# Kernel optimization log

Hardware: AMD Instinct MI355X
Metric: run time of the kernel (lower is better)

Reference implementation:

```python
import jax, jax.numpy as jnp
import numpy as np

B, S = 128, 72
ITER = 16
D_MODEL, D_INPUT = 1024, 512
MEM = 25
HEADS, DH = 8, 64
N_SO, N_SA = 256, 64
NUM_CLASSES = 1968
MH = 16
VOCAB, TED = 32, 128
SA_SZ = N_SA * (N_SA + 1) // 2  # 2080
SO_SZ = N_SO * (N_SO + 1) // 2  # 32896
I_A, J_A = np.triu_indices(N_SA)
I_O, J_O = np.triu_indices(N_SO)


def _ln(x, g, b):
    m = x.mean(-1, keepdims=True)
    v = ((x - m) ** 2).mean(-1, keepdims=True)
    return (x - m) / jnp.sqrt(v + 1e-5) * g + b


def _glu(x):
    a, g = jnp.split(x, 2, axis=-1)
    return a * jax.nn.sigmoid(g)


def setup_inputs():
    key = jax.random.key(0)
    ks = iter(jax.random.split(key, 32))

    def u(shape, s):
        return jax.random.uniform(next(ks), shape, jnp.float32, -s, s)

    return {
        "x": jax.random.randint(next(ks), (B, S), 0, VOCAB),
        "emb": u((VOCAB, TED), 1.0),
        "kv_w": u((TED, D_INPUT), (1.0 / TED) ** 0.5),
        "kv_b": jnp.zeros((D_INPUT,), jnp.float32),
        "kv_ln_g": jnp.ones((D_INPUT,), jnp.float32),
        "kv_ln_b": jnp.zeros((D_INPUT,), jnp.float32),
        "q_w": u((SA_SZ, D_INPUT), (1.0 / SA_SZ) ** 0.5),
        "q_b": jnp.zeros((D_INPUT,), jnp.float32),
        "in_proj_w": u((D_INPUT, 3 * D_INPUT), (1.0 / D_INPUT) ** 0.5),
        "in_proj_b": jnp.zeros((3 * D_INPUT,), jnp.float32),
        "out_proj_w": u((D_INPUT, D_INPUT), (1.0 / D_INPUT) ** 0.5),
        "out_proj_b": jnp.zeros((D_INPUT,), jnp.float32),
        "syn_w": u((D_INPUT + D_MODEL, 2 * D_MODEL), (1.0 / (D_INPUT + D_MODEL)) ** 0.5),
        "syn_b": jnp.zeros((2 * D_MODEL,), jnp.float32),
        "syn_ln_g": jnp.ones((D_MODEL,), jnp.float32),
        "syn_ln_b": jnp.zeros((D_MODEL,), jnp.float32),
        "tp1_w": u((MEM, 2 * MH, D_MODEL), 1.0 / (MEM + 2 * MH) ** 0.5),
        "tp1_b": jnp.zeros((1, D_MODEL, 2 * MH), jnp.float32),
        "tp2_w": u((MH, 2, D_MODEL), 1.0 / (MH + 2) ** 0.5),
        "tp2_b": jnp.zeros((1, D_MODEL, 2), jnp.float32),
        "start_act": u((D_MODEL,), (1.0 / D_MODEL) ** 0.5),
        "start_trace": u((D_MODEL, MEM), (1.0 / (D_MODEL + MEM)) ** 0.5),
        "decay_action": jnp.zeros((SA_SZ,), jnp.float32),
        "decay_out": jnp.zeros((SO_SZ,), jnp.float32),
        "out_w": u((SO_SZ, NUM_CLASSES), (1.0 / SO_SZ) ** 0.5),
        "out_b": jnp.zeros((NUM_CLASSES,), jnp.float32),
    }


def _forward(x, emb, kv_w, kv_b, kv_ln_g, kv_ln_b, q_w, q_b, in_proj_w, in_proj_b,
             out_proj_w, out_proj_b, syn_w, syn_b, syn_ln_g, syn_ln_b,
             tp1_w, tp1_b, tp2_w, tp2_b, start_act, start_trace,
             decay_action, decay_out, out_w, out_b):
    Bn = x.shape[0]
    # kv features: embed -> linear -> layernorm  (B,S,D_INPUT)
    kv = _ln(emb[x] @ kv_w + kv_b, kv_ln_g, kv_ln_b)
    Wq, Wk, Wv = jnp.split(in_proj_w, 3, axis=1)
    bq, bk, bv = jnp.split(in_proj_b, 3, axis=0)
    K = (kv @ Wk + bk).reshape(Bn, -1, HEADS, DH)  # (B,S,H,Dh)
    V = (kv @ Wv + bv).reshape(Bn, -1, HEADS, DH)
    # decayed running-sync coefficients (decay params clamped to [0,15])
    r_a = jnp.exp(-jnp.clip(decay_action, 0.0, 15.0))
    r_o = jnp.exp(-jnp.clip(decay_out, 0.0, 15.0))
    act0 = jnp.broadcast_to(start_act, (Bn, D_MODEL))
    trace0 = jnp.broadcast_to(start_trace, (Bn, D_MODEL, MEM))
    so0 = act0[:, :N_SO]
    a_o0 = so0[:, I_O] * so0[:, J_O]           # initial out-sync alpha
    b_o0 = jnp.ones_like(a_o0)
    a_a0 = jnp.zeros((Bn, SA_SZ), kv.dtype)    # None-init == zeros under update rule
    b_a0 = jnp.zeros((Bn, SA_SZ), kv.dtype)

    def step(carry, _):
        act, trace, a_a, b_a, a_o, b_o = carry
        # action synchronisation (last N_SA neurons, triu outer product)
        sa = act[:, -N_SA:]
        a_a = r_a * a_a + sa[:, I_A] * sa[:, J_A]
        b_a = r_a * b_a + 1.0
        sync_a = a_a / jnp.sqrt(b_a)
        # single-query multihead attention over kv
        q = sync_a @ q_w + q_b
        qh = (q @ Wq + bq).reshape(Bn, HEADS, DH)
        scores = jnp.einsum('bhd,bshd->bhs', qh, K) / (DH ** 0.5)
        attn = jax.nn.softmax(scores, axis=-1)
        o = jnp.einsum('bhs,bshd->bhd', attn, V).reshape(Bn, D_INPUT)
        o = o @ out_proj_w + out_proj_b
        # synapses: concat -> linear -> GLU -> layernorm
        pre = jnp.concatenate([o, act], axis=-1)
        state = _ln(_glu(pre @ syn_w + syn_b), syn_ln_g, syn_ln_b)
        # shift trace, append new state
        trace = jnp.concatenate([trace[:, :, 1:], state[:, :, None]], axis=-1)
        # per-neuron NLM: SuperLinear -> GLU -> SuperLinear -> GLU -> squeeze
        h = _glu(jnp.einsum('bdm,mhd->bdh', trace, tp1_w) + tp1_b)      # (B,D,MH)
        act = _glu(jnp.einsum('bdm,mhd->bdh', h, tp2_w) + tp2_b)[..., 0]  # (B,D)
        # out synchronisation (first N_SO neurons)
        so = act[:, :N_SO]
        a_o = r_o * a_o + so[:, I_O] * so[:, J_O]
        b_o = r_o * b_o + 1.0
        sync_o = a_o / jnp.sqrt(b_o)
        pred = sync_o @ out_w + out_b                                   # (B,C)
        lp = jax.nn.log_softmax(pred, axis=-1)
        ne = -jnp.sum(jnp.exp(lp) * lp, axis=-1) / jnp.log(jnp.float32(NUM_CLASSES))
        cert = jnp.stack([ne, 1.0 - ne], axis=-1)                       # (B,2)
        return (act, trace, a_a, b_a, a_o, b_o), (pred, cert)

    _, (preds, certs) = jax.lax.scan(step, (act0, trace0, a_a0, b_a0, a_o0, b_o0), None, length=ITER)
    predictions = jnp.moveaxis(preds, 0, -1)   # (B,C,ITER)
    certainties = jnp.moveaxis(certs, 0, -1)   # (B,2,ITER)
    return predictions, certainties


def reference(x, emb, kv_w, kv_b, kv_ln_g, kv_ln_b, q_w, q_b, in_proj_w, in_proj_b,
              out_proj_w, out_proj_b, syn_w, syn_b, syn_ln_g, syn_ln_b,
              tp1_w, tp1_b, tp2_w, tp2_b, start_act, start_trace,
              decay_action, decay_out, out_w, out_b):
    return _forward(x, emb, kv_w, kv_b, kv_ln_g, kv_ln_b, q_w, q_b, in_proj_w, in_proj_b,
                    out_proj_w, out_proj_b, syn_w, syn_b, syn_ln_g, syn_ln_b,
                    tp1_w, tp1_b, tp2_w, tp2_b, start_act, start_trace,
                    decay_action, decay_out, out_w, out_b)
```

## Files before the change

kernel.cpp:

```cpp
#include <hip/hip_runtime.h>
#include <math.h>

#define BB 128
#define SS 72
#define NITER 16
#define D_IN 512
#define D_MODEL 1024
#define MEMN 25
#define HEADS 8
#define DHH 64
#define N_SO 256
#define N_SA 64
#define SA_SZ 2080
#define SO_SZ 32896
#define NCLS 1968
#define TED 128
#define VOCAB 32
#define ROWS (BB*SS)
#define TRACE_SLOTS (MEMN + NITER)

#define BGN 64
#define BGKS 16
#define BGKLEN 2056
#define BGSTEPS 33
#define NPART 1984
#define WHLD 1984
#define WCHUNKS 124
#define SYNZ 6

typedef _Float16 half_t;
typedef _Float16 half8 __attribute__((ext_vector_type(8)));
typedef float f32x4v __attribute__((ext_vector_type(4)));

__device__ __forceinline__ float sigmoidf_(float x){ return 1.f/(1.f+expf(-x)); }

__device__ __forceinline__ float bsum256(float v, float* red){
  int tid = threadIdx.x; red[tid] = v; __syncthreads();
#pragma unroll
  for (int s = 128; s > 0; s >>= 1){ if (tid < s) red[tid] += red[tid+s]; __syncthreads(); }
  float r = red[0]; __syncthreads(); return r;
}

__device__ __forceinline__ long triu_off(int n, int i){
  return (long)i*n - ((long)i*(i-1))/2;
}

__device__ __forceinline__ int swzA(int b){ return b ^ (((b>>9)&1)<<5); }

__global__ void k_conv(const float* __restrict__ src, half_t* __restrict__ dst, int n){
  int gid = blockIdx.x*256 + threadIdx.x;
  if (gid < n) dst[gid] = (half_t)src[gid];
}

#define CV0 (VOCAB*TED)
#define CV1 (CV0 + TED*D_IN)
#define CV2 (CV1 + D_IN*D_IN)
#define CV3 (CV2 + D_IN*D_IN)
__global__ void k_convall(const float* __restrict__ emb, const float* __restrict__ kv_w,
                          const float* __restrict__ in_proj_w,
                          half_t* __restrict__ embh, half_t* __restrict__ kvwh,
                          half_t* __restrict__ Wkh, half_t* __restrict__ Wvh){
  int gid = blockIdx.x*256 + threadIdx.x;
  if (gid < CV0){ embh[gid] = (half_t)emb[gid]; return; }
  if (gid < CV1){ int i = gid - CV0; kvwh[i] = (half_t)kv_w[i]; return; }
  if (gid < CV2){ int i = gid - CV1; int r = i >> 9, c = i & 511;
                  Wkh[i] = (half_t)in_proj_w[(size_t)r*1536 + 512 + c]; return; }
  if (gid < CV3){ int i = gid - CV2; int r = i >> 9, c = i & 511;
                  Wvh[i] = (half_t)in_proj_w[(size_t)r*1536 + 1024 + c]; return; }
}

__global__ void k_convsyn(const float* __restrict__ Wf2, const float* __restrict__ syn_w,
                          half_t* __restrict__ Wsynh){
  int gid = blockIdx.x*256 + threadIdx.x;
  if (gid >= 1536*2048) return;
  Wsynh[gid] = (half_t)((gid < 512*2048) ? Wf2[gid] : syn_w[gid]);
}

__global__ void k_embed_h(const int* __restrict__ x, const half_t* __restrict__ embh,
                          half_t* __restrict__ out){
  int gid = blockIdx.x*256 + threadIdx.x;
  if (gid >= ROWS*(TED/8)) return;
  int row = gid >> 4, c0 = (gid & 15)*8;
  *(half8*)(out + (size_t)row*TED + c0) = *(const half8*)(embh + (size_t)x[row]*TED + c0);
}

__global__ void k_init_pairs(int n, int npairs, const float* __restrict__ decay,
                             int2* __restrict__ pairs, float* __restrict__ rv){
  int p = blockIdx.x*256 + threadIdx.x;
  if (p >= npairs) return;
  double nn = (double)n;
  double disc = (2.0*nn+1.0)*(2.0*nn+1.0) - 8.0*(double)p;
  int i = (int)floor(((2.0*nn+1.0) - sqrt(disc))*0.5);
  if (i < 0) i = 0; if (i > n-1) i = n-1;
  while (i+1 < n && triu_off(n, i+1) <= (long)p) i++;
  while (i > 0 && triu_off(n, i) > (long)p) i--;
  int j = i + (int)((long)p - triu_off(n, i));
  pairs[p] = make_int2(i, j);
  float dc = decay[p]; dc = fminf(fmaxf(dc, 0.f), 15.f);
  rv[p] = expf(-dc);
}

__global__ void k_init_act(const float* __restrict__ sa, float* __restrict__ act,
                           half_t* __restrict__ Ah16){
  int gid = blockIdx.x*256 + threadIdx.x;
  if (gid >= BB*D_MODEL) return;
  int b = gid >> 10, d = gid & 1023;
  float v = sa[d];
  act[gid] = v;
  Ah16[(size_t)b*1536 + 512 + d] = (half_t)v;
}

__global__ void k_zero(float* __restrict__ p, int n){
  int gid = blockIdx.x*256 + threadIdx.x;
  if (gid < n) p[gid] = 0.f;
}

__global__ void k_init_trace(const float* __restrict__ st, float* __restrict__ trace){
  int gid = blockIdx.x*256 + threadIdx.x;
  if (gid >= BB*MEMN*D_MODEL) return;
  int d = gid & 1023;
  int m = (gid >> 10) % MEMN;
  int b = (gid >> 10) / MEMN;
  trace[(size_t)b*TRACE_SLOTS*D_MODEL + (size_t)m*D_MODEL + d] = st[d*MEMN + m];
}

__global__ void k_init_ao(const float* __restrict__ sa, const int2* __restrict__ pairs,
                          float* __restrict__ ao){
  int p = blockIdx.x*256 + threadIdx.x;
  if (p >= SO_SZ) return;
  int b = blockIdx.y;
  int2 ij = pairs[p];
  ao[(size_t)b*SO_SZ + p] = sa[ij.x]*sa[ij.y];
}

__global__ void k_convw(const float* __restrict__ W, half_t* __restrict__ Wh){
  int gid = blockIdx.x*256 + threadIdx.x;
  if (gid >= SO_SZ*WCHUNKS) return;
  int row = gid / WCHUNKS, ch = gid - row*WCHUNKS;
  int c0 = ch*16;
  half_t* dst = Wh + (size_t)row*WHLD + c0;
  if (ch < 123){
    const float4* src = (const float4*)(W + (size_t)row*NCLS + c0);
    float4 f0 = src[0], f1 = src[1], f2 = src[2], f3 = src[3];
    half8 h0, h1;
    h0[0]=(half_t)f0.x; h0[1]=(half_t)f0.y; h0[2]=(half_t)f0.z; h0[3]=(half_t)f0.w;
    h0[4]=(half_t)f1.x; h0[5]=(half_t)f1.y; h0[6]=(half_t)f1.z; h0[7]=(half_t)f1.w;
    h1[0]=(half_t)f2.x; h1[1]=(half_t)f2.y; h1[2]=(half_t)f2.z; h1[3]=(half_t)f2.w;
    h1[4]=(half_t)f3.x; h1[5]=(half_t)f3.y; h1[6]=(half_t)f3.z; h1[7]=(half_t)f3.w;
    *(half8*)dst = h0; *(half8*)(dst+8) = h1;
  } else {
    half8 zz;
#pragma unroll
    for (int j = 0; j < 8; j++) zz[j] = (half_t)0.f;
    *(half8*)dst = zz; *(half8*)(dst+8) = zz;
  }
}

__global__ void k_colsum(const float* __restrict__ vec, const float* __restrict__ W,
                         int ldw, const float* __restrict__ addb,
                         float* __restrict__ out, int N, int K){
  int col = blockIdx.x*256 + threadIdx.x;
  if (col >= N) return;
  float s = addb ? addb[col] : 0.f;
  for (int k = 0; k < K; k++) s = fmaf(vec[k], W[(size_t)k*ldw + col], s);
  out[col] = s;
}

template<int MB>
__global__ void k_gemm(const float* __restrict__ A, int lda,
                       const float* __restrict__ W, int ldw, int wrow0, int wcol0,
                       const float* __restrict__ bias,
                       float* __restrict__ C, int ldc, int N, int K){
  constexpr int KC = 32;
  const int tid = threadIdx.x;
  const int col = blockIdx.x*256 + tid;
  const int row0 = blockIdx.y*MB;
  __shared__ float As[MB][KC];
  float acc[MB];
#pragma unroll
  for (int r = 0; r < MB; r++) acc[r] = 0.f;
  for (int kk = 0; kk < K; kk += KC){
    __syncthreads();
    for (int idx = tid; idx < MB*KC; idx += 256){
      int r = idx / KC, k = idx % KC;
      As[r][k] = A[(size_t)(row0+r)*lda + kk + k];
    }
    __syncthreads();
#pragma unroll
    for (int k = 0; k < KC; k++){
      float w = W[(size_t)(wrow0+kk+k)*ldw + wcol0 + col];
#pragma unroll
      for (int r = 0; r < MB; r++) acc[r] = fmaf(As[r][k], w, acc[r]);
    }
  }
#pragma unroll
  for (int r = 0; r < MB; r++){
    size_t o = (size_t)(row0+r)*ldc + col;
    C[o] = acc[r] + (bias ? bias[col] : 0.f);
  }
}

__global__ __launch_bounds__(256)
void k_pgemm(const half_t* __restrict__ Ah, int ldah,
             const half_t* __restrict__ Wh16, const float* __restrict__ bias,
             float* __restrict__ C, int ksteps){
  __shared__ half_t As[2][128*64];
  __shared__ half_t Ws[2][64*66];
  const int tid = threadIdx.x;
  const int nb0 = blockIdx.x * 64;
  const int row0 = blockIdx.y * 128;
  const int l = tid & 63, wv = tid >> 6;
  const int mw = (wv >> 1) * 64, nw = (wv & 1) * 32;
  const int c = l & 15, g = l >> 4;

  f32x4v acc[4][2];
#pragma unroll
  for (int i = 0; i < 4; i++)
#pragma unroll
    for (int j2 = 0; j2 < 2; j2++)
#pragma unroll
      for (int r = 0; r < 4; r++) acc[i][j2][r] = 0.f;

  auto stage = [&](int s, int buf){
#pragma unroll
    for (int it = 0; it < 4; it++){
      int ch = tid + it*256;
      int m = ch >> 3, kl = (ch & 7)*8;
      half8 v = *(const half8*)(Ah + (size_t)(row0+m)*ldah + s*64 + kl);
      *(half8*)((char*)(&As[buf][0]) + swzA(ch*16)) = v;
    }
    {
      int k = tid >> 2, cs = (tid & 3) * 16;
      const half_t* wr = Wh16 + (size_t)(s*64 + k) * D_IN + nb0 + cs;
      char* dst = (char*)(&Ws[buf][0]) + (size_t)(k*66 + cs) * 2;
      union { half8 v; unsigned int u[4]; } p0, p1;
      p0.v = *(const half8*)wr; p1.v = *(const half8*)(wr + 8);
#pragma unroll
      for (int q = 0; q < 4; q++){
        ((unsigned int*)dst)[q]        = p0.u[q];
        ((unsigned int*)(dst + 16))[q] = p1.u[q];
      }
    }
  };

  stage(0, 0);
  __syncthreads();
  for (int s = 0; s < ksteps; s++){
    int buf = s & 1;
    if (s + 1 < ksteps) stage(s+1, buf^1);
#pragma unroll
    for (int h = 0; h < 2; h++){
      half8 a8[4];
#pragma unroll
      for (int mb = 0; mb < 4; mb++)
        a8[mb] = *(const half8*)((const char*)(&As[buf][0]) +
                   swzA(((mw + mb*16 + c)*64 + h*32 + g*8)*2));
#pragma unroll
      for (int nb = 0; nb < 2; nb++){
        half8 b8;
        const half_t* wp = &Ws[buf][(h*32 + g*8)*66 + nw + nb*16 + c];
#pragma unroll
        for (int j = 0; j < 8; j++) b8[j] = wp[j*66];
#pragma unroll
        for (int mb = 0; mb < 4; mb++)
          acc[mb][nb] = __builtin_amdgcn_mfma_f32_16x16x32_f16(a8[mb], b8, acc[mb][nb], 0, 0, 0);
      }
    }
    __syncthreads();
  }
#pragma unroll
  for (int mb = 0; mb < 4; mb++)
#pragma unroll
    for (int nb = 0; nb < 2; nb++){
      int m = mw + mb*16 + g*4;
      int n = nb0 + nw + nb*16 + c;
      float bv = bias[n];
#pragma unroll
      for (int r = 0; r < 4; r++)
        C[(size_t)(row0 + m + r) * D_IN + n] = acc[mb][nb][r] + bv;
    }
}

__global__ __launch_bounds__(256)
void k_syn16(const half_t* __restrict__ Ah, const half_t* __restrict__ Wh16,
             float* __restrict__ outp){
  __shared__ half_t As[2][128*64];
  __shared__ half_t Ws[2][64*66];
  const int tid = threadIdx.x;
  const int nb0 = blockIdx.x * 64;
  const int z = blockIdx.y;
  const int l = tid & 63, wv = tid >> 6;
  const int mw = (wv >> 1) * 64, nw = (wv & 1) * 32;
  const int c = l & 15, g = l >> 4;
  const int kbase = z * 256;

  f32x4v acc[4][2];
#pragma unroll
  for (int i = 0; i < 4; i++)
#pragma unroll
    for (int j2 = 0; j2 < 2; j2++)
#pragma unroll
      for (int r = 0; r < 4; r++) acc[i][j2][r] = 0.f;

  auto stage = [&](int s, int buf){
#pragma unroll
    for (int it = 0; it < 4; it++){
      int ch = tid + it*256;
      int m = ch >> 3, kl = (ch & 7)*8;
      half8 v = *(const half8*)(Ah + (size_t)m*1536 + kbase + s*64 + kl);
      *(half8*)((char*)(&As[buf][0]) + swzA(ch*16)) = v;
    }
    {
      int k = tid >> 2, cs = (tid & 3) * 16;
      const half_t* wr = Wh16 + (size_t)(kbase + s*64 + k) * 2048 + nb0 + cs;
      char* dst = (char*)(&Ws[buf][0]) + (size_t)(k*66 + cs) * 2;
      union { half8 v; unsigned int u[4]; } p0, p1;
      p0.v = *(const half8*)wr; p1.v = *(const half8*)(wr + 8);
#pragma unroll
      for (int q = 0; q < 4; q++){
        ((unsigned int*)dst)[q]        = p0.u[q];
        ((unsigned int*)(dst + 16))[q] = p1.u[q];
      }
    }
  };

  stage(0, 0);
  __syncthreads();
  for (int s = 0; s < 4; s++){
    int buf = s & 1;
    if (s + 1 < 4) stage(s+1, buf^1);
#pragma unroll
    for (int h = 0; h < 2; h++){
      half8 a8[4];
#pragma unroll
      for (int mb = 0; mb < 4; mb++)
        a8[mb] = *(const half8*)((const char*)(&As[buf][0]) +
                   swzA(((mw + mb*16 + c)*64 + h*32 + g*8)*2));
#pragma unroll
      for (int nb = 0; nb < 2; nb++){
        half8 b8;
        const half_t* wp = &Ws[buf][(h*32 + g*8)*66 + nw + nb*16 + c];
#pragma unroll
        for (int j = 0; j < 8; j++) b8[j] = wp[j*66];
#pragma unroll
        for (int mb = 0; mb < 4; mb++)
          acc[mb][nb] = __builtin_amdgcn_mfma_f32_16x16x32_f16(a8[mb], b8, acc[mb][nb], 0, 0, 0);
      }
    }
    __syncthreads();
  }
  float* pz = outp + (size_t)z * BB * 2048;
#pragma unroll
  for (int mb = 0; mb < 4; mb++)
#pragma unroll
    for (int nb = 0; nb < 2; nb++){
      int m = mw + mb*16 + g*4;
      int n = nb0 + nw + nb*16 + c;
#pragma unroll
      for (int r = 0; r < 4; r++)
        pz[(size_t)(m + r) * 2048 + n] = acc[mb][nb][r];
    }
}

__global__ void k_gemmq(const float* __restrict__ act,
                        const float* __restrict__ r_a, const int2* __restrict__ pairsA,
                        const float* __restrict__ aaIn, float* __restrict__ aaOut,
                        const half_t* __restrict__ Wh, float* __restrict__ qpart, int t){
  constexpr int KC = 32;
  const int tid = threadIdx.x;
  const int col = blockIdx.x*256 + tid;
  const int row0 = blockIdx.y*4;
  const int z = blockIdx.z;
  const int kstart = z*544;
  const int kend = min(SA_SZ, kstart + 544);
  const bool writer = (blockIdx.x == 0);
  __shared__ float As[4][KC];
  float acc[4] = {0.f,0.f,0.f,0.f};
  for (int kk = kstart; kk < kend; kk += KC){
    __syncthreads();
    if (tid < 4*KC){
      int r = tid >> 5, k = tid & 31;
      int p = kk + k;
      int b = row0 + r;
      int2 ij = pairsA[p];
      const float* ab = act + (size_t)b*D_MODEL + (D_MODEL - N_SA);
      float rv = r_a[p];
      size_t idx = (size_t)b*SA_SZ + p;
      float a = fmaf(rv, aaIn[idx], ab[ij.x]*ab[ij.y]);
      if (writer) aaOut[idx] = a;
      float bb = 0.f;
      for (int i = 0; i <= t; i++) bb = fmaf(rv, bb, 1.f);
      As[r][k] = a / sqrtf(bb);
    }
    __syncthreads();
#pragma unroll
    for (int k = 0; k < KC; k++){
      float w = (float)Wh[(size_t)(kk+k)*D_IN + col];
#pragma unroll
      for (int r = 0; r < 4; r++) acc[r] = fmaf(As[r][k], w, acc[r]);
    }
  }
#pragma unroll
  for (int r = 0; r < 4; r++)
    qpart[(size_t)z*BB*D_IN + (size_t)(row0+r)*D_IN + col] = acc[r];
}

__global__ void k_gemm2srcZ(const float* __restrict__ A1, const float* __restrict__ A2,
                            const float* __restrict__ W1, const float* __restrict__ W2,
                            float* __restrict__ outp){
  constexpr int MB = 8, KC = 32;
  const int tid = threadIdx.x;
  const int col = blockIdx.x*256 + tid;
  const int row0 = blockIdx.y*MB;
  const int z = blockIdx.z;
  __shared__ float As[MB][KC];
  float acc[MB];
#pragma unroll
  for (int r = 0; r < MB; r++) acc[r] = 0.f;
  for (int kk = z*256; kk < z*256 + 256; kk += KC){
    __syncthreads();
    for (int idx = tid; idx < MB*KC; idx += 256){
      int r = idx / KC, k = idx % KC;
      int kg = kk + k;
      As[r][k] = (kg < D_IN) ? A1[(size_t)(row0+r)*D_IN + kg]
                             : A2[(size_t)(row0+r)*D_MODEL + kg - D_IN];
    }
    __syncthreads();
    const float* Wp = (kk < D_IN) ? W1 : W2;
#pragma unroll
    for (int k = 0; k < KC; k++){
      float w = Wp[(size_t)(kk+k)*2048 + col];
#pragma unroll
      for (int r = 0; r < MB; r++) acc[r] = fmaf(As[r][k], w, acc[r]);
    }
  }
#pragma unroll
  for (int r = 0; r < MB; r++)
    outp[(size_t)z*BB*2048 + (size_t)(row0+r)*2048 + col] = acc[r];
}

__global__ void k_ln_h(const float* __restrict__ X, const float* __restrict__ g,
                       const float* __restrict__ bta, half_t* __restrict__ Y, int D){
  const int row = blockIdx.x, tid = threadIdx.x;
  __shared__ float red[256];
  const float* xr = X + (size_t)row*D;
  float s = 0.f;
  for (int c = tid; c < D; c += 256) s += xr[c];
  float mean = bsum256(s, red) / (float)D;
  float s2 = 0.f;
  for (int c = tid; c < D; c += 256){ float d = xr[c]-mean; s2 += d*d; }
  float var = bsum256(s2, red) / (float)D;
  float inv = 1.f / sqrtf(var + 1e-5f);
  half_t* yr = Y + (size_t)row*D;
  for (int c = tid; c < D; c += 256) yr[c] = (half_t)((xr[c]-mean)*inv*g[c] + bta[c]);
}

__global__ void k_glu_ln(const float* __restrict__ synpart, const float* __restrict__ bias2,
                         const float* __restrict__ g, const float* __restrict__ bta,
                         float* __restrict__ traceSlot){
  const int b = blockIdx.x, tid = threadIdx.x;
  __shared__ float vals[D_MODEL];
  __shared__ float red[256];
  for (int c = tid; c < 1024; c += 256){
    float a = bias2[c], gg = bias2[c+1024];
#pragma unroll
    for (int z = 0; z < SYNZ; z++){
      const float* sp = synpart + (size_t)z*BB*2048 + (size_t)b*2048;
      a  += sp[c];
      gg += sp[c+1024];
    }
    vals[c] = a * sigmoidf_(gg);
  }
  __syncthreads();
  float s = 0.f;
  for (int c = tid; c < 1024; c += 256) s += vals[c];
  float mean = bsum256(s, red) * (1.f/1024.f);
  float s2 = 0.f;
  for (int c = tid; c < 1024; c += 256){ float d = vals[c]-mean; s2 += d*d; }
  float var = bsum256(s2, red) * (1.f/1024.f);
  float inv = 1.f / sqrtf(var + 1e-5f);
  float* out = traceSlot + (size_t)b*(TRACE_SLOTS*D_MODEL);
  for (int c = tid; c < 1024; c += 256) out[c] = (vals[c]-mean)*inv*g[c] + bta[c];
}

__global__ void k_attn(const float* __restrict__ qpart, const float* __restrict__ bqf,
                       const float* __restrict__ Km, const float* __restrict__ Vm,
                       float* __restrict__ o, half_t* __restrict__ Ah16){
  const int bh = blockIdx.x, b = bh >> 3, h = bh & 7;
  const int tid = threadIdx.x;
  __shared__ float qs[DHH];
  __shared__ float attn[SS];
  __shared__ float red[128];
  if (tid < DHH){
    int d = h*DHH + tid;
    float qv = bqf[d];
#pragma unroll
    for (int z = 0; z < 4; z++) qv += qpart[(size_t)z*BB*D_IN + (size_t)b*D_IN + d];
    qs[tid] = qv;
  }
  __syncthreads();
  float sc = -1e30f;
  if (tid < SS){
    const float* kp = Km + ((size_t)(b*SS+tid)*HEADS + h)*DHH;
    float d = 0.f;
#pragma unroll
    for (int i = 0; i < DHH; i++) d = fmaf(qs[i], kp[i], d);
    sc = d * 0.125f;
  }
  red[tid] = sc; __syncthreads();
  for (int s2 = 64; s2 > 0; s2 >>= 1){ if (tid < s2) red[tid] = fmaxf(red[tid], red[tid+s2]); __syncthreads(); }
  float m = red[0]; __syncthreads();
  float e = (tid < SS) ? expf(sc - m) : 0.f;
  red[tid] = e; __syncthreads();
  for (int s2 = 64; s2 > 0; s2 >>= 1){ if (tid < s2) red[tid] += red[tid+s2]; __syncthreads(); }
  float inv = 1.f / red[0]; __syncthreads();
  if (tid < SS) attn[tid] = e * inv;
  __syncthreads();
  if (tid < DHH){
    const float* vp = Vm + ((size_t)(b*SS)*HEADS + h)*DHH + tid;
    float acc = 0.f;
    for (int s2 = 0; s2 < SS; s2++) acc = fmaf(attn[s2], vp[(size_t)s2*D_IN], acc);
    int d = h*DHH + tid;
    o[(size_t)b*D_IN + d] = acc;
    Ah16[(size_t)b*1536 + d] = (half_t)acc;
  }
}

__global__ void k_neuron(const float* __restrict__ trace,
                         const float* __restrict__ tp1w, const float* __restrict__ tp1b,
                         const float* __restrict__ tp2w, const float* __restrict__ tp2b,
                         float* __restrict__ act, half_t* __restrict__ Ah16, int t){
  int gid = blockIdx.x*256 + threadIdx.x;
  if (gid >= BB*D_MODEL) return;
  int b = gid >> 10, d = gid & 1023;
  const float* tr = trace + (size_t)b*(TRACE_SLOTS*D_MODEL) + (size_t)(t+1)*D_MODEL + d;
  float trv[MEMN];
#pragma unroll
  for (int m = 0; m < MEMN; m++) trv[m] = tr[(size_t)m*D_MODEL];
  float o0 = tp2b[d*2+0], o1 = tp2b[d*2+1];
#pragma unroll
  for (int j = 0; j < 16; j++){
    const float* wpj = tp1w + (size_t)j*1024 + d;
    const float* wpg = tp1w + (size_t)(j+16)*1024 + d;
    float hj = tp1b[d*32 + j];
    float hg = tp1b[d*32 + j + 16];
#pragma unroll
    for (int m = 0; m < MEMN; m++){
      float tv = trv[m];
      hj = fmaf(tv, wpj[(size_t)m*32*1024], hj);
      hg = fmaf(tv, wpg[(size_t)m*32*1024], hg);
    }
    float hgv = hj * sigmoidf_(hg);
    o0 = fmaf(hgv, tp2w[(size_t)(j*2+0)*1024 + d], o0);
    o1 = fmaf(hgv, tp2w[(size_t)(j*2+1)*1024 + d], o1);
  }
  float v = o0 * sigmoidf_(o1);
  act[gid] = v;
  Ah16[(size_t)b*1536 + 512 + d] = (half_t)v;
}

__global__ void k_syncO(const float* __restrict__ act, const float* __restrict__ rv,
                        const int2* __restrict__ pairs, float* __restrict__ ao,
                        half_t* __restrict__ syncv, int t){
  int p = blockIdx.x*256 + threadIdx.x;
  if (p >= SO_SZ) return;
  int b = blockIdx.y;
  int2 ij = pairs[p];
  const float* ab = act + (size_t)b*D_MODEL;
  float r = rv[p];
  size_t idx = (size_t)b*SO_SZ + p;
  float a = fmaf(r, ao[idx], ab[ij.x]*ab[ij.y]);
  ao[idx] = a;
  float bb = 1.f;
  for (int i = 0; i <= t; i++) bb = fmaf(r, bb, 1.f);
  syncv[idx] = (half_t)(a / sqrtf(bb));
}

__global__ __launch_bounds__(256)
void k_bigemm2h(const half_t* __restrict__ Ah, const half_t* __restrict__ Wh,
                float* __restrict__ part){
  __shared__ half_t As[2][128*64];
  __shared__ half_t Ws[2][64*66];
  const int tid = threadIdx.x;
  const int z = blockIdx.y;
  const int nb0 = blockIdx.x * BGN;
  const int l = tid & 63, wv = tid >> 6;
  const int mw = (wv >> 1) * 64, nw = (wv & 1) * 32;
  const int c = l & 15, g = l >> 4;
  const int k0 = z * BGKLEN;

  f32x4v acc[4][2];
#pragma unroll
  for (int i = 0; i < 4; i++)
#pragma unroll
    for (int j2 = 0; j2 < 2; j2++)
#pragma unroll
      for (int r = 0; r < 4; r++) acc[i][j2][r] = 0.f;

  auto stage = [&](int s, int buf){
    const int kv = min(64, BGKLEN - s*64);
#pragma unroll
    for (int it = 0; it < 4; it++){
      int ch = tid + it*256;
      int m = ch >> 3, kg = ch & 7, kl = kg*8;
      half8 v;
      if (kl < kv) v = *(const half8*)(Ah + (size_t)m*SO_SZ + k0 + s*64 + kl);
      else {
#pragma unroll
        for (int j = 0; j < 8; j++) v[j] = (half_t)0.f;
      }
      *(half8*)((char*)(&As[buf][0]) + swzA(ch*16)) = v;
    }
    {
      int k = tid >> 2, cs = (tid & 3) * 16;
      const half_t* wr = Wh + (size_t)(k0 + s*64 + k) * WHLD + nb0 + cs;
      char* dst = (char*)(&Ws[buf][0]) + (size_t)(k*66 + cs) * 2;
      union { half8 v; unsigned int u[4]; } p0, p1;
      if (k < kv){ p0.v = *(const half8*)wr; p1.v = *(const half8*)(wr + 8); }
      else {
#pragma unroll
        for (int j = 0; j < 8; j++){ p0.v[j] = (half_t)0.f; p1.v[j] = (half_t)0.f; }
      }
#pragma unroll
      for (int q = 0; q < 4; q++){
        ((unsigned int*)dst)[q]        = p0.u[q];
        ((unsigned int*)(dst + 16))[q] = p1.u[q];
      }
    }
  };

  stage(0, 0);
  __syncthreads();
  for (int s = 0; s < BGSTEPS; s++){
    int buf = s & 1;
    if (s + 1 < BGSTEPS) stage(s+1, buf^1);
#pragma unroll
    for (int h = 0; h < 2; h++){
      half8 a8[4];
#pragma unroll
      for (int mb = 0; mb < 4; mb++)
        a8[mb] = *(const half8*)((const char*)(&As[buf][0]) +
                   swzA(((mw + mb*16 + c)*64 + h*32 + g*8)*2));
#pragma unroll
      for (int nb = 0; nb < 2; nb++){
        half8 b8;
        const half_t* wp = &Ws[buf][(h*32 + g*8)*66 + nw + nb*16 + c];
#pragma unroll
        for (int j = 0; j < 8; j++) b8[j] = wp[j*66];
#pragma unroll
        for (int mb = 0; mb < 4; mb++)
          acc[mb][nb] = __builtin_amdgcn_mfma_f32_16x16x32_f16(a8[mb], b8, acc[mb][nb], 0, 0, 0);
      }
    }
    __syncthreads();
  }
  float* pz = part + (size_t)z * 128 * NPART;
#pragma unroll
  for (int mb = 0; mb < 4; mb++)
#pragma unroll
    for (int nb = 0; nb < 2; nb++){
      int m = mw + mb*16 + g*4;
      int n = nb0 + nw + nb*16 + c;
#pragma unroll
      for (int r = 0; r < 4; r++)
        pz[(size_t)(m + r) * NPART + n] = acc[mb][nb][r];
    }
}

__global__ void k_output(const float* __restrict__ part, const float* __restrict__ outb,
                         float* __restrict__ dout, int t){
  const int b = blockIdx.x, tid = threadIdx.x;
  __shared__ float pred[NCLS];
  __shared__ float red[256];
  float lmax = -1e30f;
  for (int c = tid; c < NCLS; c += 256){
    float s = outb[c];
    const float* pp = part + (size_t)b*NPART + c;
#pragma unroll
    for (int z = 0; z < BGKS; z++) s += pp[(size_t)z*128*NPART];
    pred[c] = s;
    dout[((size_t)b*NCLS + c)*NITER + t] = s;
    lmax = fmaxf(lmax, s);
  }
  red[tid] = lmax; __syncthreads();
  for (int s2 = 128; s2 > 0; s2 >>= 1){ if (tid < s2) red[tid] = fmaxf(red[tid], red[tid+s2]); __syncthreads(); }
  float m = red[0]; __syncthreads();
  float se = 0.f;
  for (int c = tid; c < NCLS; c += 256) se += expf(pred[c]-m);
  float Z = bsum256(se, red);
  float logZ = m + logf(Z);
  float ent = 0.f;
  for (int c = tid; c < NCLS; c += 256){ float lp = pred[c]-logZ; ent += expf(lp)*lp; }
  float E = bsum256(ent, red);
  if (tid == 0){
    float ne = -E * (1.f/logf((float)NCLS));
    float* cp = dout + (size_t)BB*NCLS*NITER + (size_t)b*2*NITER + t;
    cp[0]     = ne;
    cp[NITER] = 1.f - ne;
  }
}

extern "C" void kernel_launch(void* const* d_in, const int* in_sizes, int n_in,
                              void* d_out, int out_size, void* d_ws, size_t ws_size,
                              hipStream_t stream){
  const int*   x           = (const int*)  d_in[0];
  const float* emb         = (const float*)d_in[1];
  const float* kv_w        = (const float*)d_in[2];
  const float* kv_b        = (const float*)d_in[3];
  const float* kv_ln_g     = (const float*)d_in[4];
  const float* kv_ln_b     = (const float*)d_in[5];
  const float* q_w         = (const float*)d_in[6];
  const float* q_b         = (const float*)d_in[7];
  const float* in_proj_w   = (const float*)d_in[8];
  const float* in_proj_b   = (const float*)d_in[9];
  const float* out_proj_w  = (const float*)d_in[10];
  const float* out_proj_b  = (const float*)d_in[11];
  const float* syn_w       = (const float*)d_in[12];
  const float* syn_b       = (const float*)d_in[13];
  const float* syn_ln_g    = (const float*)d_in[14];
  const float* syn_ln_b    = (const float*)d_in[15];
  const float* tp1_w       = (const float*)d_in[16];
  const float* tp1_b       = (const float*)d_in[17];
  const float* tp2_w       = (const float*)d_in[18];
  const float* tp2_b       = (const float*)d_in[19];
  const float* start_act   = (const float*)d_in[20];
  const float* start_trace = (const float*)d_in[21];
  const float* decay_action= (const float*)d_in[22];
  const float* decay_out   = (const float*)d_in[23];
  const float* out_w       = (const float*)d_in[24];
  const float* out_b       = (const float*)d_in[25];
  float* dout = (float*)d_out;

  float* w = (float*)d_ws;
  size_t off = 0;
  auto alloc = [&](size_t n){ n = (n + 3) & ~(size_t)3; float* p = w + off; off += n; return p; };
  float* region0 = alloc((size_t)BGKS*128*NPART);
  float* region1 = alloc((size_t)ROWS*D_IN);
  float* Kmat    = alloc((size_t)ROWS*D_IN);
  float* Vmat    = alloc((size_t)ROWS*D_IN);
  float* trace   = alloc((size_t)BB*TRACE_SLOTS*D_MODEL);
  half_t* sync_oh= (half_t*)alloc((size_t)BB*SO_SZ/2);
  float* a_aP    = alloc((size_t)2*BB*SA_SZ);
  float* act     = alloc((size_t)BB*D_MODEL);
  float* qpart   = alloc((size_t)4*BB*D_IN);
  float* obuf    = alloc((size_t)BB*D_IN);
  float* qfw     = alloc((size_t)SA_SZ*D_IN);
  float* Wf2     = alloc((size_t)D_IN*2048);
  float* bqf     = alloc(D_IN);
  float* bias2   = alloc(2048);
  float* r_a     = alloc(SA_SZ);
  float* r_o     = alloc(SO_SZ);
  int2*  pairsA  = (int2*)alloc(2*SA_SZ);
  int2*  pairsO  = (int2*)alloc(2*SO_SZ);
  half_t* embh   = (half_t*)alloc((size_t)VOCAB*TED/2);
  half_t* kvwh   = (half_t*)alloc((size_t)TED*D_IN/2);
  half_t* Wkh    = (half_t*)alloc((size_t)D_IN*D_IN/2);
  half_t* Wvh    = (half_t*)alloc((size_t)D_IN*D_IN/2);
  half_t* qfwh   = (half_t*)alloc((size_t)SA_SZ*D_IN/2);
  half_t* Wh     = (half_t*)alloc(((size_t)SO_SZ*WHLD)/2);
  half_t* Ah16   = (half_t*)alloc((size_t)BB*1536/2);
  half_t* Wsynh  = (half_t*)alloc((size_t)1536*2048/2);
  const bool use_syn16 = (off * sizeof(float) <= ws_size);

  half_t* embx_h = (half_t*)region0;
  half_t* kvh    = (half_t*)region0;
  float* part    = region0;
  float* synpart = region0;
  float* kvbuf = region1;
  float* a_o   = region1;

  dim3 blk(256);

  k_convall<<<(CV3+255)/256, blk, 0, stream>>>(emb, kv_w, in_proj_w, embh, kvwh, Wkh, Wvh);
  k_embed_h<<<(ROWS*(TED/8)+255)/256, blk, 0, stream>>>(x, embh, embx_h);
  k_pgemm<<<dim3(8, ROWS/128), blk, 0, stream>>>(embx_h, TED, kvwh, kv_b, kvbuf, TED/64);
  k_ln_h<<<ROWS, blk, 0, stream>>>(kvbuf, kv_ln_g, kv_ln_b, kvh, D_IN);
  k_pgemm<<<dim3(8, ROWS/128), blk, 0, stream>>>(kvh, D_IN, Wkh, in_proj_b+512,  Kmat, D_IN/64);
  k_pgemm<<<dim3(8, ROWS/128), blk, 0, stream>>>(kvh, D_IN, Wvh, in_proj_b+1024, Vmat, D_IN/64);
  k_gemm<4><<<dim3(2, SA_SZ/4), blk, 0, stream>>>(q_w, D_IN, in_proj_w, 1536, 0, 0, nullptr, qfw, D_IN, D_IN, D_IN);
  k_gemm<4><<<dim3(8, D_IN/4), blk, 0, stream>>>(out_proj_w, D_IN, syn_w, 2048, 0, 0, nullptr, Wf2, 2048, 2048, D_IN);
  k_conv<<<(SA_SZ*D_IN+255)/256, blk, 0, stream>>>(qfw, qfwh, SA_SZ*D_IN);
  k_colsum<<<2, blk, 0, stream>>>(q_b, in_proj_w, 1536, in_proj_b, bqf, D_IN, D_IN);
  k_colsum<<<8, blk, 0, stream>>>(out_proj_b, syn_w, 2048, syn_b, bias2, 2048, D_IN);
  k_convw<<<(SO_SZ*WCHUNKS+255)/256, blk, 0, stream>>>(out_w, Wh);
  if (use_syn16)
    k_convsyn<<<(1536*2048+255)/256, blk, 0, stream>>>(Wf2, syn_w, Wsynh);
  k_init_pairs<<<(SA_SZ+255)/256, blk, 0, stream>>>(N_SA, SA_SZ, decay_action, pairsA, r_a);
  k_init_pairs<<<(SO_SZ+255)/256, blk, 0, stream>>>(N_SO, SO_SZ, decay_out,    pairsO, r_o);
  k_init_act<<<(BB*D_MODEL+255)/256, blk, 0, stream>>>(start_act, act, Ah16);
  k_zero<<<(2*BB*SA_SZ+255)/256, blk, 0, stream>>>(a_aP, 2*BB*SA_SZ);
  k_init_trace<<<(BB*MEMN*D_MODEL+255)/256, blk, 0, stream>>>(start_trace, trace);
  k_init_ao<<<dim3((SO_SZ+255)/256, BB), blk, 0, stream>>>(start_act, pairsO, a_o);

  for (int t = 0; t < NITER; t++){
    float* aaIn  = a_aP + (size_t)(t & 1)*BB*SA_SZ;
    float* aaOut = a_aP + (size_t)((t+1) & 1)*BB*SA_SZ;
    k_gemmq<<<dim3(2, 32, 4), blk, 0, stream>>>(act, r_a, pairsA, aaIn, aaOut, qfwh, qpart, t);
    k_attn<<<BB*HEADS, 128, 0, stream>>>(qpart, bqf, Kmat, Vmat, obuf, Ah16);
    if (use_syn16)
      k_syn16<<<dim3(32, SYNZ), blk, 0, stream>>>(Ah16, Wsynh, synpart);
    else
      k_gemm2srcZ<<<dim3(8, 16, SYNZ), blk, 0, stream>>>(obuf, act, Wf2, syn_w, synpart);
    k_glu_ln<<<BB, blk, 0, stream>>>(synpart, bias2, syn_ln_g, syn_ln_b, trace + (size_t)(MEMN+t)*D_MODEL);
    k_neuron<<<(BB*D_MODEL+255)/256, blk, 0, stream>>>(trace, tp1_w, tp1_b, tp2_w, tp2_b, act, Ah16, t);
    k_syncO<<<dim3((SO_SZ+255)/256, BB), blk, 0, stream>>>(act, r_o, pairsO, a_o, sync_oh, t);
    k_bigemm2h<<<dim3(31, BGKS), blk, 0, stream>>>(sync_oh, Wh, part);
    k_output<<<BB, blk, 0, stream>>>(part, out_b, dout, t);
  }
}
```

Baseline: 2.993 ms.

## Move weight-folding GEMMs to fp16 MFMA kernel and split column sums over K

Replaces the scalar fp32 k_gemm used to fold q_w·Wq and out_proj_w·syn_w with the existing MFMA fp16 k_pgemm. The kernel is generalized with ldw/ldc parameters and an optional bias, and q_w is zero-padded to a multiple of 128 rows. The serial column-sum bias kernels are split into a K-partitioned partial pass plus a reduction, which gives them more parallelism. The folded weights now come from fp16 inputs, so some precision is lost, and the conversion kernel does extra work.

```diff
diff --git a/kernel.cpp b/kernel.cpp
--- a/kernel.cpp
+++ b/kernel.cpp
@@ -18,6 +18,7 @@
 #define VOCAB 32
 #define ROWS (BB*SS)
 #define TRACE_SLOTS (MEMN + NITER)
+#define QPAD 2176
 
 #define BGN 64
 #define BGKS 16
@@ -56,10 +57,18 @@
 #define CV1 (CV0 + TED*D_IN)
 #define CV2 (CV1 + D_IN*D_IN)
 #define CV3 (CV2 + D_IN*D_IN)
+#define CV4 (CV3 + D_IN*D_IN)
+#define CV5 (CV4 + D_IN*D_IN)
+#define CV6 (CV5 + D_IN*2048)
+#define CV7 (CV6 + QPAD*D_IN)
 __global__ void k_convall(const float* __restrict__ emb, const float* __restrict__ kv_w,
                           const float* __restrict__ in_proj_w,
+                          const float* __restrict__ out_proj_w,
+                          const float* __restrict__ syn_w, const float* __restrict__ q_w,
                           half_t* __restrict__ embh, half_t* __restrict__ kvwh,
-                          half_t* __restrict__ Wkh, half_t* __restrict__ Wvh){
+                          half_t* __restrict__ Wkh, half_t* __restrict__ Wvh,
+                          half_t* __restrict__ Wqh, half_t* __restrict__ oph,
+                          half_t* __restrict__ synth, half_t* __restrict__ qwh){
   int gid = blockIdx.x*256 + threadIdx.x;
   if (gid < CV0){ embh[gid] = (half_t)emb[gid]; return; }
   if (gid < CV1){ int i = gid - CV0; kvwh[i] = (half_t)kv_w[i]; return; }
@@ -67,6 +76,12 @@
                   Wkh[i] = (half_t)in_proj_w[(size_t)r*1536 + 512 + c]; return; }
   if (gid < CV3){ int i = gid - CV2; int r = i >> 9, c = i & 511;
                   Wvh[i] = (half_t)in_proj_w[(size_t)r*1536 + 1024 + c]; return; }
+  if (gid < CV4){ int i = gid - CV3; int r = i >> 9, c = i & 511;
+                  Wqh[i] = (half_t)in_proj_w[(size_t)r*1536 + c]; return; }
+  if (gid < CV5){ int i = gid - CV4; oph[i] = (half_t)out_proj_w[i]; return; }
+  if (gid < CV6){ int i = gid - CV5; synth[i] = (half_t)syn_w[i]; return; }
+  if (gid < CV7){ int i = gid - CV6; int r = i >> 9;
+                  qwh[i] = (r < SA_SZ) ? (half_t)q_w[i] : (half_t)0.f; return; }
 }
 
 __global__ void k_convsyn(const float* __restrict__ Wf2, const float* __restrict__ syn_w,
@@ -156,54 +171,32 @@
   }
 }
 
-__global__ void k_colsum(const float* __restrict__ vec, const float* __restrict__ W,
-                         int ldw, const float* __restrict__ addb,
-                         float* __restrict__ out, int N, int K){
+__global__ void k_colsumP(const float* __restrict__ vec, const float* __restrict__ W,
+                          int ldw, float* __restrict__ part, int N){
+  int col = blockIdx.x*256 + threadIdx.x;
+  int kz = blockIdx.y;
+  if (col >= N) return;
+  float s = 0.f;
+#pragma unroll
+  for (int k = kz*32; k < kz*32 + 32; k++)
+    s = fmaf(vec[k], W[(size_t)k*ldw + col], s);
+  part[(size_t)kz*N + col] = s;
+}
+
+__global__ void k_colsumR(const float* __restrict__ part, const float* __restrict__ addb,
+                          float* __restrict__ out, int N){
   int col = blockIdx.x*256 + threadIdx.x;
   if (col >= N) return;
-  float s = addb ? addb[col] : 0.f;
-  for (int k = 0; k < K; k++) s = fmaf(vec[k], W[(size_t)k*ldw + col], s);
+  float s = addb[col];
+#pragma unroll
+  for (int z = 0; z < 16; z++) s += part[(size_t)z*N + col];
   out[col] = s;
-}
-
-template<int MB>
-__global__ void k_gemm(const float* __restrict__ A, int lda,
-                       const float* __restrict__ W, int ldw, int wrow0, int wcol0,
-                       const float* __restrict__ bias,
-                       float* __restrict__ C, int ldc, int N, int K){
-  constexpr int KC = 32;
-  const int tid = threadIdx.x;
-  const int col = blockIdx.x*256 + tid;
-  const int row0 = blockIdx.y*MB;
-  __shared__ float As[MB][KC];
-  float acc[MB];
-#pragma unroll
-  for (int r = 0; r < MB; r++) acc[r] = 0.f;
-  for (int kk = 0; kk < K; kk += KC){
-    __syncthreads();
-    for (int idx = tid; idx < MB*KC; idx += 256){
-      int r = idx / KC, k = idx % KC;
-      As[r][k] = A[(size_t)(row0+r)*lda + kk + k];
-    }
-    __syncthreads();
-#pragma unroll
-    for (int k = 0; k < KC; k++){
-      float w = W[(size_t)(wrow0+kk+k)*ldw + wcol0 + col];
-#pragma unroll
-      for (int r = 0; r < MB; r++) acc[r] = fmaf(As[r][k], w, acc[r]);
-    }
-  }
-#pragma unroll
-  for (int r = 0; r < MB; r++){
-    size_t o = (size_t)(row0+r)*ldc + col;
-    C[o] = acc[r] + (bias ? bias[col] : 0.f);
-  }
 }
 
 __global__ __launch_bounds__(256)
 void k_pgemm(const half_t* __restrict__ Ah, int ldah,
-             const half_t* __restrict__ Wh16, const float* __restrict__ bias,
-             float* __restrict__ C, int ksteps){
+             const half_t* __restrict__ Wh16, int ldw, const float* __restrict__ bias,
+             float* __restrict__ C, int ldc, int ksteps){
   __shared__ half_t As[2][128*64];
   __shared__ half_t Ws[2][64*66];
   const int tid = threadIdx.x;
@@ -231,7 +224,7 @@
     }
     {
       int k = tid >> 2, cs = (tid & 3) * 16;
-      const half_t* wr = Wh16 + (size_t)(s*64 + k) * D_IN + nb0 + cs;
+      const half_t* wr = Wh16 + (size_t)(s*64 + k) * ldw + nb0 + cs;
       char* dst = (char*)(&Ws[buf][0]) + (size_t)(k*66 + cs) * 2;
       union { half8 v; unsigned int u[4]; } p0, p1;
       p0.v = *(const half8*)wr; p1.v = *(const half8*)(wr + 8);
@@ -274,10 +267,10 @@
     for (int nb = 0; nb < 2; nb++){
       int m = mw + mb*16 + g*4;
       int n = nb0 + nw + nb*16 + c;
-      float bv = bias[n];
+      float bv = bias ? bias[n] : 0.f;
 #pragma unroll
       for (int r = 0; r < 4; r++)
-        C[(size_t)(row0 + m + r) * D_IN + n] = acc[mb][nb][r] + bv;
+        C[(size_t)(row0 + m + r) * ldc + n] = acc[mb][nb][r] + bv;
     }
 }
 
@@ -744,10 +737,11 @@
   float* act     = alloc((size_t)BB*D_MODEL);
   float* qpart   = alloc((size_t)4*BB*D_IN);
   float* obuf    = alloc((size_t)BB*D_IN);
-  float* qfw     = alloc((size_t)SA_SZ*D_IN);
+  float* qfwPad  = alloc((size_t)QPAD*D_IN);
   float* Wf2     = alloc((size_t)D_IN*2048);
   float* bqf     = alloc(D_IN);
   float* bias2   = alloc(2048);
+  float* colpart = alloc((size_t)16*2048);
   float* r_a     = alloc(SA_SZ);
   float* r_o     = alloc(SO_SZ);
   int2*  pairsA  = (int2*)alloc(2*SA_SZ);
@@ -756,6 +750,10 @@
   half_t* kvwh   = (half_t*)alloc((size_t)TED*D_IN/2);
   half_t* Wkh    = (half_t*)alloc((size_t)D_IN*D_IN/2);
   half_t* Wvh    = (half_t*)alloc((size_t)D_IN*D_IN/2);
+  half_t* Wqh    = (half_t*)alloc((size_t)D_IN*D_IN/2);
+  half_t* oph    = (half_t*)alloc((size_t)D_IN*D_IN/2);
+  half_t* synth  = (half_t*)alloc((size_t)D_IN*2048/2);
+  half_t* qwh    = (half_t*)alloc((size_t)QPAD*D_IN/2);
   half_t* qfwh   = (half_t*)alloc((size_t)SA_SZ*D_IN/2);
   half_t* Wh     = (half_t*)alloc(((size_t)SO_SZ*WHLD)/2);
   half_t* Ah16   = (half_t*)alloc((size_t)BB*1536/2);
@@ -771,17 +769,20 @@
 
   dim3 blk(256);
 
-  k_convall<<<(CV3+255)/256, blk, 0, stream>>>(emb, kv_w, in_proj_w, embh, kvwh, Wkh, Wvh);
+  k_convall<<<(CV7+255)/256, blk, 0, stream>>>(emb, kv_w, in_proj_w, out_proj_w, syn_w, q_w,
+                                               embh, kvwh, Wkh, Wvh, Wqh, oph, synth, qwh);
   k_embed_h<<<(ROWS*(TED/8)+255)/256, blk, 0, stream>>>(x, embh, embx_h);
-  k_pgemm<<<dim3(8, ROWS/128), blk, 0, stream>>>(embx_h, TED, kvwh, kv_b, kvbuf, TED/64);
+  k_pgemm<<<dim3(8, ROWS/128), blk, 0, stream>>>(embx_h, TED, kvwh, D_IN, kv_b, kvbuf, D_IN, TED/64);
   k_ln_h<<<ROWS, blk, 0, stream>>>(kvbuf, kv_ln_g, kv_ln_b, kvh, D_IN);
-  k_pgemm<<<dim3(8, ROWS/128), blk, 0, stream>>>(kvh, D_IN, Wkh, in_proj_b+512,  Kmat, D_IN/64);
-  k_pgemm<<<dim3(8, ROWS/128), blk, 0, stream>>>(kvh, D_IN, Wvh, in_proj_b+1024, Vmat, D_IN/64);
-  k_gemm<4><<<dim3(2, SA_SZ/4), blk, 0, stream>>>(q_w, D_IN, in_proj_w, 1536, 0, 0, nullptr, qfw, D_IN, D_IN, D_IN);
-  k_gemm<4><<<dim3(8, D_IN/4), blk, 0, stream>>>(out_proj_w, D_IN, syn_w, 2048, 0, 0, nullptr, Wf2, 2048, 2048, D_IN);
-  k_conv<<<(SA_SZ*D_IN+255)/256, blk, 0, stream>>>(qfw, qfwh, SA_SZ*D_IN);
-  k_colsum<<<2, blk, 0, stream>>>(q_b, in_proj_w, 1536, in_proj_b, bqf, D_IN, D_IN);
-  k_colsum<<<8, blk, 0, stream>>>(out_proj_b, syn_w, 2048, syn_b, bias2, 2048, D_IN);
+  k_pgemm<<<dim3(8, ROWS/128), blk, 0, stream>>>(kvh, D_IN, Wkh, D_IN, in_proj_b+512,  Kmat, D_IN, D_IN/64);
+  k_pgemm<<<dim3(8, ROWS/128), blk, 0, stream>>>(kvh, D_IN, Wvh, D_IN, in_proj_b+1024, Vmat, D_IN, D_IN/64);
+  k_pgemm<<<dim3(8, QPAD/128), blk, 0, stream>>>(qwh, D_IN, Wqh, D_IN, nullptr, qfwPad, D_IN, D_IN/64);
+  k_pgemm<<<dim3(32, D_IN/128), blk, 0, stream>>>(oph, D_IN, synth, 2048, nullptr, Wf2, 2048, D_IN/64);
+  k_conv<<<(SA_SZ*D_IN+255)/256, blk, 0, stream>>>(qfwPad, qfwh, SA_SZ*D_IN);
+  k_colsumP<<<dim3(2, 16), blk, 0, stream>>>(q_b, in_proj_w, 1536, colpart, D_IN);
+  k_colsumR<<<2, blk, 0, stream>>>(colpart, in_proj_b, bqf, D_IN);
+  k_colsumP<<<dim3(8, 16), blk, 0, stream>>>(out_proj_b, syn_w, 2048, colpart, 2048);
+  k_colsumR<<<8, blk, 0, stream>>>(colpart, syn_b, bias2, 2048);
   k_convw<<<(SO_SZ*WCHUNKS+255)/256, blk, 0, stream>>>(out_w, Wh);
   if (use_syn16)
     k_convsyn<<<(1536*2048+255)/256, blk, 0, stream>>>(Wf2, syn_w, Wsynh);
```

Result: faster. 2.813 ms (-6.0%).
